# Optimization experiments

Measured on AMD Instinct MI355X. Metric: run time of the kernel, lower is better.

Reference implementation:

```python
import jax, jax.numpy as jnp
import numpy as np

N = 30000      # nodes
E = 480000     # edges (before self loops)
NFEAT = 128
H = 16         # heads
C = 32         # per-head channels = nhid
NCLASS = 10
G = 64         # graphs in batch
ATT_SLOPE = 0.2   # GATv2Conv negative_slope default
ACT_SLOPE = 0.01  # F.leaky_relu default


def setup_inputs() -> dict:
    key = jax.random.key(0)
    ks = jax.random.split(key, 16)
    def glorot(k, shape):
        fan = sum(shape[:2]) if len(shape) > 1 else shape[0]
        return jax.random.normal(k, shape, jnp.float32) * (2.0 / fan) ** 0.5
    inp = {
        "x": jax.random.normal(ks[0], (N, NFEAT), jnp.float32),
        # layer 1: lin_l / lin_r map NFEAT -> H*C, attention vector att [H, C]
        "Wl1": glorot(ks[1], (NFEAT, H * C)), "bl1": jnp.zeros((H * C,), jnp.float32),
        "Wr1": glorot(ks[2], (NFEAT, H * C)), "br1": jnp.zeros((H * C,), jnp.float32),
        "att1": glorot(ks[3], (H, C)), "b1": jnp.zeros((C,), jnp.float32),
        # layer 2: nhid(=C) -> H*C
        "Wl2": glorot(ks[4], (C, H * C)), "bl2": jnp.zeros((H * C,), jnp.float32),
        "Wr2": glorot(ks[5], (C, H * C)), "br2": jnp.zeros((H * C,), jnp.float32),
        "att2": glorot(ks[6], (H, C)), "b2": jnp.zeros((C,), jnp.float32),
        # classifier nhid -> nclass
        "Wc": glorot(ks[7], (C, NCLASS)), "bc": jnp.zeros((NCLASS,), jnp.float32),
        "edge_index": jax.random.randint(ks[8], (2, E), 0, N, jnp.int32),
        "batch": jnp.sort(jax.random.randint(ks[9], (N,), 0, G, jnp.int32)),
    }
    return inp


def _gatv2_layer(x, Wl, bl, Wr, br, att, b, src, dst, n):
    # GATv2Conv, concat=False (mean over heads), eval mode (no dropout)
    xl = (x @ Wl + bl).reshape(n, H, C)   # messages (x_j)
    xr = (x @ Wr + br).reshape(n, H, C)   # query side (x_i)
    e = jax.nn.leaky_relu(xl[src] + xr[dst], ATT_SLOPE)      # [E', H, C]
    score = jnp.einsum('ehc,hc->eh', e, att)                 # [E', H]
    # segment softmax over incoming edges of each dst node
    m = jax.ops.segment_max(score, dst, num_segments=n)
    ex = jnp.exp(score - m[dst])
    denom = jax.ops.segment_sum(ex, dst, num_segments=n)
    alpha = ex / denom[dst]                                  # [E', H]
    out = jax.ops.segment_sum(alpha[:, :, None] * xl[src], dst, num_segments=n)
    return out.mean(axis=1) + b                              # [n, C]


def reference(x, Wl1, bl1, Wr1, br1, att1, b1, Wl2, bl2, Wr2, br2, att2, b2, Wc, bc, edge_index, batch):
    # add self loops (PyG GATv2Conv default add_self_loops=True)
    loop = jnp.arange(N, dtype=edge_index.dtype)
    src = jnp.concatenate([edge_index[0], loop])
    dst = jnp.concatenate([edge_index[1], loop])

    h = jax.nn.leaky_relu(_gatv2_layer(x, Wl1, bl1, Wr1, br1, att1, b1, src, dst, N), ACT_SLOPE)
    h = jax.nn.leaky_relu(_gatv2_layer(h, Wl2, bl2, Wr2, br2, att2, b2, src, dst, N), ACT_SLOPE)
    # dropout is identity in eval mode
    # global mean pool over graphs
    summed = jax.ops.segment_sum(h, batch, num_segments=G)               # [G, C]
    counts = jax.ops.segment_sum(jnp.ones((N,), h.dtype), batch, num_segments=G)
    pooled = summed / jnp.maximum(counts, 1.0)[:, None]
    logits = pooled @ Wc + bc
    return logits / 1.0  # temperature = 1.0
```

## Files before the change

### kernel.cpp

```cpp
#include <hip/hip_runtime.h>
#include <float.h>

#define NNODES 30000
#define NEDGES 480000
#define NFEATK 128
#define NH 16
#define NC 32
#define HC 512
#define NCLASSES 10
#define NG 64
#define CAP 96

using half4 = __attribute__((ext_vector_type(4))) _Float16;
using half8 = __attribute__((ext_vector_type(8))) _Float16;
using f32x4 = __attribute__((ext_vector_type(4))) float;

__global__ void prep0_kernel(const float* __restrict__ x, _Float16* __restrict__ xh,
                             const float* __restrict__ Wl1, const float* __restrict__ Wr1,
                             _Float16* __restrict__ Wlt1, _Float16* __restrict__ Wrt1,
                             const float* __restrict__ Wl2, const float* __restrict__ Wr2,
                             _Float16* __restrict__ Wlt2, _Float16* __restrict__ Wrt2,
                             int* __restrict__ cnt, int* __restrict__ csr) {
    int gtid = blockIdx.x * blockDim.x + threadIdx.x;
    int gstride = gridDim.x * blockDim.x;
    for (int i = gtid; i < NNODES * NFEATK / 4; i += gstride) {
        float4 v = *(const float4*)&x[i * 4];
        half4 h = {(_Float16)v.x, (_Float16)v.y, (_Float16)v.z, (_Float16)v.w};
        *(half4*)&xh[i * 4] = h;
    }
    for (int i = gtid; i < 2 * 512 * NFEATK; i += gstride) {
        int sel = i >= 512 * NFEATK;
        int idx = i - sel * 512 * NFEATK;
        const float* W = sel ? Wr1 : Wl1;
        _Float16* Wt = sel ? Wrt1 : Wlt1;
        int n = idx & 511, k = idx >> 9;
        Wt[n * NFEATK + k] = (_Float16)W[idx];
    }
    for (int i = gtid; i < 2 * 512 * NC; i += gstride) {
        int sel = i >= 512 * NC;
        int idx = i - sel * 512 * NC;
        const float* W = sel ? Wr2 : Wl2;
        _Float16* Wt = sel ? Wrt2 : Wlt2;
        int n = idx & 511, k = idx >> 9;
        Wt[n * NC + k] = (_Float16)W[idx];
    }
    for (int i = gtid; i < NNODES; i += gstride) {
        cnt[i] = 1;
        csr[i * CAP] = i;
    }
}

__global__ void scatter_kernel(const int* __restrict__ src, const int* __restrict__ dst,
                               int* __restrict__ cnt, int* __restrict__ csr) {
    int e = blockIdx.x * blockDim.x + threadIdx.x;
    if (e >= NEDGES) return;
    int s = src[e], d = dst[e];
    int pos = atomicAdd(&cnt[d], 1);
    csr[d * CAP + pos] = s;
}

template <int K>
__launch_bounds__(256)
__global__ void dual_gemm_kernel(const _Float16* __restrict__ A,
                                 const _Float16* __restrict__ Wlt, const _Float16* __restrict__ Wrt,
                                 const float* __restrict__ bl, const float* __restrict__ br,
                                 _Float16* __restrict__ Yl, _Float16* __restrict__ Yr) {
    constexpr int Kc = K / 8;
    constexpr int AH = 64 * K;
    constexpr int BH = 128 * K;
    constexpr int YSH = 64 * 136;
    constexpr int SMEMH = (AH + BH > YSH) ? (AH + BH) : YSH;
    __shared__ __align__(16) _Float16 smem[SMEMH];
    _Float16* as = smem;
    _Float16* bs = smem + AH;

    int tid = threadIdx.x;
    int sel = blockIdx.y >> 2;
    int nbase = (blockIdx.y & 3) * 128;
    const _Float16* Bt = sel ? Wrt : Wlt;
    const float* bias = sel ? br : bl;
    _Float16* Y = sel ? Yr : Yl;
    int mb = blockIdx.x;

    for (int c = tid; c < 64 * Kc; c += 256) {
        int row = c / Kc, k8 = c % Kc;
        int arow = mb * 64 + row; if (arow > NNODES - 1) arow = NNODES - 1;
        half8 v = *(const half8*)&A[(size_t)arow * K + k8 * 8];
        *(half8*)&as[(row * Kc + (k8 ^ (row & (Kc - 1)))) * 8] = v;
    }
    for (int c = tid; c < 128 * Kc; c += 256) {
        int row = c / Kc, k8 = c % Kc;
        half8 v = *(const half8*)&Bt[(size_t)(nbase + row) * K + k8 * 8];
        *(half8*)&bs[(row * Kc + (k8 ^ (row & (Kc - 1)))) * 8] = v;
    }
    __syncthreads();

    int wave = tid >> 6, lane = tid & 63;
    int quad = lane >> 4, l16 = lane & 15;
    int am = l16 & (Kc - 1);

    f32x4 acc[8];
    #pragma unroll
    for (int f = 0; f < 8; f++) acc[f] = (f32x4){0.f, 0.f, 0.f, 0.f};

    #pragma unroll
    for (int kk = 0; kk < Kc; kk += 4) {
        int k8 = (kk + quad) ^ am;
        half8 a = *(const half8*)&as[((wave * 16 + l16) * Kc + k8) * 8];
        #pragma unroll
        for (int f = 0; f < 8; f++) {
            half8 b = *(const half8*)&bs[((f * 16 + l16) * Kc + k8) * 8];
            acc[f] = __builtin_amdgcn_mfma_f32_16x16x32_f16(a, b, acc[f], 0, 0, 0);
        }
    }
    __syncthreads();

    _Float16* ys = smem;
    #pragma unroll
    for (int f = 0; f < 8; f++) {
        float bv = bias[nbase + f * 16 + l16];
        #pragma unroll
        for (int r = 0; r < 4; r++) {
            ys[(wave * 16 + quad * 4 + r) * 136 + f * 16 + l16] = (_Float16)(acc[f][r] + bv);
        }
    }
    __syncthreads();
    int mtop = mb * 64;
    for (int c = tid; c < 64 * 16; c += 256) {
        int r = c >> 4, cc = (c & 15) * 8;
        int grow = mtop + r;
        if (grow < NNODES)
            *(half8*)&Y[(size_t)grow * HC + nbase + cc] = *(half8*)&ys[r * 136 + cc];
    }
}

template <typename OUT>
__launch_bounds__(128)
__global__ void gat_edge_kernel(const _Float16* __restrict__ xlh, const _Float16* __restrict__ xrh,
                                const float* __restrict__ att, const float* __restrict__ bvec,
                                const int* __restrict__ cnt, const int* __restrict__ csr_src,
                                OUT* __restrict__ hout) {
    int d = blockIdx.x;
    int t = threadIdx.x;
    int col = t * 4;
    half4 xrq = *(const half4*)&xrh[(size_t)d * HC + col];
    float4 xrv = {(float)xrq.x, (float)xrq.y, (float)xrq.z, (float)xrq.w};
    float4 attv = *(const float4*)&att[col];
    int beg = d * CAP, end = beg + cnt[d];

    float l = 0.f;
    float a0 = 0.f, a1 = 0.f, a2 = 0.f, a3 = 0.f;
    for (int i = beg; i < end; i += 4) {
        int n = end - i;
        int s0 = csr_src[i];
        int s1 = csr_src[n > 1 ? i + 1 : i];
        int s2 = csr_src[n > 2 ? i + 2 : i];
        int s3 = csr_src[n > 3 ? i + 3 : i];
        half4 q0 = *(const half4*)&xlh[(size_t)s0 * HC + col];
        half4 q1 = *(const half4*)&xlh[(size_t)s1 * HC + col];
        half4 q2 = *(const half4*)&xlh[(size_t)s2 * HC + col];
        half4 q3 = *(const half4*)&xlh[(size_t)s3 * HC + col];
        float x00 = (float)q0.x, x01 = (float)q0.y, x02 = (float)q0.z, x03 = (float)q0.w;
        float x10 = (float)q1.x, x11 = (float)q1.y, x12 = (float)q1.z, x13 = (float)q1.w;
        float x20 = (float)q2.x, x21 = (float)q2.y, x22 = (float)q2.z, x23 = (float)q2.w;
        float x30 = (float)q3.x, x31 = (float)q3.y, x32 = (float)q3.z, x33 = (float)q3.w;

        float e, v0, v1, v2, v3;
        e = x00 + xrv.x; e = (e > 0.f) ? e : 0.2f * e; v0  = e * attv.x;
        e = x01 + xrv.y; e = (e > 0.f) ? e : 0.2f * e; v0 += e * attv.y;
        e = x02 + xrv.z; e = (e > 0.f) ? e : 0.2f * e; v0 += e * attv.z;
        e = x03 + xrv.w; e = (e > 0.f) ? e : 0.2f * e; v0 += e * attv.w;
        e = x10 + xrv.x; e = (e > 0.f) ? e : 0.2f * e; v1  = e * attv.x;
        e = x11 + xrv.y; e = (e > 0.f) ? e : 0.2f * e; v1 += e * attv.y;
        e = x12 + xrv.z; e = (e > 0.f) ? e : 0.2f * e; v1 += e * attv.z;
        e = x13 + xrv.w; e = (e > 0.f) ? e : 0.2f * e; v1 += e * attv.w;
        e = x20 + xrv.x; e = (e > 0.f) ? e : 0.2f * e; v2  = e * attv.x;
        e = x21 + xrv.y; e = (e > 0.f) ? e : 0.2f * e; v2 += e * attv.y;
        e = x22 + xrv.z; e = (e > 0.f) ? e : 0.2f * e; v2 += e * attv.z;
        e = x23 + xrv.w; e = (e > 0.f) ? e : 0.2f * e; v2 += e * attv.w;
        e = x30 + xrv.x; e = (e > 0.f) ? e : 0.2f * e; v3  = e * attv.x;
        e = x31 + xrv.y; e = (e > 0.f) ? e : 0.2f * e; v3 += e * attv.y;
        e = x32 + xrv.z; e = (e > 0.f) ? e : 0.2f * e; v3 += e * attv.z;
        e = x33 + xrv.w; e = (e > 0.f) ? e : 0.2f * e; v3 += e * attv.w;

        #pragma unroll
        for (int off = 1; off < 8; off <<= 1) {
            v0 += __shfl_xor(v0, off);
            v1 += __shfl_xor(v1, off);
            v2 += __shfl_xor(v2, off);
            v3 += __shfl_xor(v3, off);
        }
        float p0 = __expf(v0);
        float p1 = (n > 1) ? __expf(v1) : 0.f;
        float p2 = (n > 2) ? __expf(v2) : 0.f;
        float p3 = (n > 3) ? __expf(v3) : 0.f;
        l += (p0 + p1) + (p2 + p3);
        a0 += p0 * x00 + p1 * x10 + p2 * x20 + p3 * x30;
        a1 += p0 * x01 + p1 * x11 + p2 * x21 + p3 * x31;
        a2 += p0 * x02 + p1 * x12 + p2 * x22 + p3 * x32;
        a3 += p0 * x03 + p1 * x13 + p2 * x23 + p3 * x33;
    }
    float inv = 1.0f / l;
    float4 o = {a0 * inv, a1 * inv, a2 * inv, a3 * inv};

    __shared__ float red[512];
    *(float4*)&red[col] = o;
    __syncthreads();
    if (t < 32) {
        float ssum = 0.f;
        #pragma unroll
        for (int hh = 0; hh < NH; ++hh) ssum += red[hh * 32 + t];
        float r = ssum * (1.0f / (float)NH) + bvec[t];
        r = (r > 0.f) ? r : 0.01f * r;
        hout[d * NC + t] = (OUT)r;
    }
}

__launch_bounds__(1024)
__global__ void pool_classify_kernel(const float* __restrict__ h, const int* __restrict__ batch,
                                     const float* __restrict__ Wc, const float* __restrict__ bc,
                                     float* __restrict__ out) {
    int g = blockIdx.x;
    int lo = 0, hi = NNODES;
    while (lo < hi) { int mid = (lo + hi) >> 1; if (batch[mid] < g) lo = mid + 1; else hi = mid; }
    int start = lo;
    hi = NNODES;
    while (lo < hi) { int mid = (lo + hi) >> 1; if (batch[mid] <= g) lo = mid + 1; else hi = mid; }
    int endn = lo;
    int cntg = endn - start;

    int tid = threadIdx.x;
    int c = tid & 31, nl = tid >> 5;
    float s = 0.f;
    for (int n = start + nl; n < endn; n += 32) s += h[n * NC + c];
    __shared__ float red[1024];
    red[tid] = s;
    __syncthreads();
    if (tid < 32) {
        float t = 0.f;
        #pragma unroll
        for (int j = 0; j < 32; j++) t += red[j * 32 + tid];
        red[tid] = t / fmaxf((float)cntg, 1.0f);
    }
    __syncthreads();
    if (tid < NCLASSES) {
        float sum = bc[tid];
        #pragma unroll
        for (int cc = 0; cc < NC; cc++) sum += red[cc] * Wc[cc * NCLASSES + tid];
        out[g * NCLASSES + tid] = sum;
    }
}


extern "C" void kernel_launch(void* const* d_in, const int* in_sizes, int n_in,
                              void* d_out, int out_size, void* d_ws, size_t ws_size,
                              hipStream_t stream) {
    const float* x    = (const float*)d_in[0];
    const float* Wl1  = (const float*)d_in[1];
    const float* bl1  = (const float*)d_in[2];
    const float* Wr1  = (const float*)d_in[3];
    const float* br1  = (const float*)d_in[4];
    const float* att1 = (const float*)d_in[5];
    const float* b1   = (const float*)d_in[6];
    const float* Wl2  = (const float*)d_in[7];
    const float* bl2  = (const float*)d_in[8];
    const float* Wr2  = (const float*)d_in[9];
    const float* br2  = (const float*)d_in[10];
    const float* att2 = (const float*)d_in[11];
    const float* b2   = (const float*)d_in[12];
    const float* Wc   = (const float*)d_in[13];
    const float* bc   = (const float*)d_in[14];
    const int* ei     = (const int*)d_in[15];
    const int* batch  = (const int*)d_in[16];
    float* out = (float*)d_out;

    const int* srcp = ei;
    const int* dstp = ei + NEDGES;

    char* ws = (char*)d_ws;
    size_t off = 0;
    auto alloc = [&](size_t bytes) -> void* {
        void* p = ws + off;
        off += (bytes + 255) & ~(size_t)255;
        return p;
    };
    _Float16* xlh  = (_Float16*)alloc(sizeof(_Float16) * (size_t)NNODES * HC);
    _Float16* xrh  = (_Float16*)alloc(sizeof(_Float16) * (size_t)NNODES * HC);
    _Float16* xh   = (_Float16*)alloc(sizeof(_Float16) * (size_t)NNODES * NFEATK);
    _Float16* h1   = (_Float16*)alloc(sizeof(_Float16) * (size_t)NNODES * NC);
    float* h2      = (float*)alloc(sizeof(float) * (size_t)NNODES * NC);
    _Float16* Wlt1 = (_Float16*)alloc(sizeof(_Float16) * 512 * NFEATK);
    _Float16* Wrt1 = (_Float16*)alloc(sizeof(_Float16) * 512 * NFEATK);
    _Float16* Wlt2 = (_Float16*)alloc(sizeof(_Float16) * 512 * NC);
    _Float16* Wrt2 = (_Float16*)alloc(sizeof(_Float16) * 512 * NC);
    int*   cnt     = (int*)alloc(sizeof(int) * NNODES);
    int*   csr     = (int*)alloc(sizeof(int) * (size_t)NNODES * CAP);

    prep0_kernel<<<512, 256, 0, stream>>>(x, xh, Wl1, Wr1, Wlt1, Wrt1,
                                          Wl2, Wr2, Wlt2, Wrt2, cnt, csr);
    scatter_kernel<<<(NEDGES + 255) / 256, 256, 0, stream>>>(srcp, dstp, cnt, csr);

    const int MB = (NNODES + 63) / 64;

    dual_gemm_kernel<NFEATK><<<dim3(MB, 8), 256, 0, stream>>>(xh, Wlt1, Wrt1, bl1, br1, xlh, xrh);
    gat_edge_kernel<_Float16><<<NNODES, 128, 0, stream>>>(xlh, xrh, att1, b1, cnt, csr, h1);

    dual_gemm_kernel<NC><<<dim3(MB, 8), 256, 0, stream>>>(h1, Wlt2, Wrt2, bl2, br2, xlh, xrh);
    gat_edge_kernel<float><<<NNODES, 128, 0, stream>>>(xlh, xrh, att2, b2, cnt, csr, h2);

    pool_classify_kernel<<<NG, 1024, 0, stream>>>(h2, batch, Wc, bc, out);
}
```

Measured before the change: 323.1 us.

## Merge edge scatter into prep, fold self-loops in-register, fuse pooling via atomics

```diff
diff --git a/kernel.cpp b/kernel.cpp
--- a/kernel.cpp
+++ b/kernel.cpp
@@ -11,18 +11,32 @@
 #define NG 64
 #define CAP 96
 
+#define CONV_BLOCKS 512
+#define SCAT_BLOCKS 1875
+
 using half4 = __attribute__((ext_vector_type(4))) _Float16;
 using half8 = __attribute__((ext_vector_type(8))) _Float16;
 using f32x4 = __attribute__((ext_vector_type(4))) float;
 
-__global__ void prep0_kernel(const float* __restrict__ x, _Float16* __restrict__ xh,
-                             const float* __restrict__ Wl1, const float* __restrict__ Wr1,
-                             _Float16* __restrict__ Wlt1, _Float16* __restrict__ Wrt1,
-                             const float* __restrict__ Wl2, const float* __restrict__ Wr2,
-                             _Float16* __restrict__ Wlt2, _Float16* __restrict__ Wrt2,
-                             int* __restrict__ cnt, int* __restrict__ csr) {
-    int gtid = blockIdx.x * blockDim.x + threadIdx.x;
-    int gstride = gridDim.x * blockDim.x;
+__global__ void prep_kernel(const float* __restrict__ x, _Float16* __restrict__ xh,
+                            const float* __restrict__ Wl1, const float* __restrict__ Wr1,
+                            _Float16* __restrict__ Wlt1, _Float16* __restrict__ Wrt1,
+                            const float* __restrict__ Wl2, const float* __restrict__ Wr2,
+                            _Float16* __restrict__ Wlt2, _Float16* __restrict__ Wrt2,
+                            const int* __restrict__ src, const int* __restrict__ dst,
+                            int* __restrict__ cnt, int* __restrict__ csr) {
+    int bid = blockIdx.x, tid = threadIdx.x;
+    if (bid >= CONV_BLOCKS) {
+        int e = (bid - CONV_BLOCKS) * 256 + tid;
+        if (e < NEDGES) {
+            int s = src[e], d = dst[e];
+            int pos = atomicAdd(&cnt[d], 1);
+            csr[d * CAP + pos] = s;
+        }
+        return;
+    }
+    int gtid = bid * 256 + tid;
+    const int gstride = CONV_BLOCKS * 256;
     for (int i = gtid; i < NNODES * NFEATK / 4; i += gstride) {
         float4 v = *(const float4*)&x[i * 4];
         half4 h = {(_Float16)v.x, (_Float16)v.y, (_Float16)v.z, (_Float16)v.w};
@@ -44,19 +58,6 @@
         int n = idx & 511, k = idx >> 9;
         Wt[n * NC + k] = (_Float16)W[idx];
     }
-    for (int i = gtid; i < NNODES; i += gstride) {
-        cnt[i] = 1;
-        csr[i * CAP] = i;
-    }
-}
-
-__global__ void scatter_kernel(const int* __restrict__ src, const int* __restrict__ dst,
-                               int* __restrict__ cnt, int* __restrict__ csr) {
-    int e = blockIdx.x * blockDim.x + threadIdx.x;
-    if (e >= NEDGES) return;
-    int s = src[e], d = dst[e];
-    int pos = atomicAdd(&cnt[d], 1);
-    csr[d * CAP + pos] = s;
 }
 
 template <int K>
@@ -134,12 +135,13 @@
     }
 }
 
-template <typename OUT>
+template <bool POOL, typename OUT>
 __launch_bounds__(128)
 __global__ void gat_edge_kernel(const _Float16* __restrict__ xlh, const _Float16* __restrict__ xrh,
                                 const float* __restrict__ att, const float* __restrict__ bvec,
                                 const int* __restrict__ cnt, const int* __restrict__ csr_src,
-                                OUT* __restrict__ hout) {
+                                const int* __restrict__ batch,
+                                OUT* __restrict__ hout, float* __restrict__ pool) {
     int d = blockIdx.x;
     int t = threadIdx.x;
     int col = t * 4;
@@ -148,8 +150,21 @@
     float4 attv = *(const float4*)&att[col];
     int beg = d * CAP, end = beg + cnt[d];
 
-    float l = 0.f;
-    float a0 = 0.f, a1 = 0.f, a2 = 0.f, a3 = 0.f;
+    float l, a0, a1, a2, a3;
+    {
+        half4 q = *(const half4*)&xlh[(size_t)d * HC + col];
+        float x0 = (float)q.x, x1 = (float)q.y, x2 = (float)q.z, x3 = (float)q.w;
+        float e, v;
+        e = x0 + xrv.x; e = (e > 0.f) ? e : 0.2f * e; v  = e * attv.x;
+        e = x1 + xrv.y; e = (e > 0.f) ? e : 0.2f * e; v += e * attv.y;
+        e = x2 + xrv.z; e = (e > 0.f) ? e : 0.2f * e; v += e * attv.z;
+        e = x3 + xrv.w; e = (e > 0.f) ? e : 0.2f * e; v += e * attv.w;
+        #pragma unroll
+        for (int off = 1; off < 8; off <<= 1) v += __shfl_xor(v, off);
+        float p = __expf(v);
+        l = p; a0 = p * x0; a1 = p * x1; a2 = p * x2; a3 = p * x3;
+    }
+
     for (int i = beg; i < end; i += 4) {
         int n = end - i;
         int s0 = csr_src[i];
@@ -212,43 +227,31 @@
         for (int hh = 0; hh < NH; ++hh) ssum += red[hh * 32 + t];
         float r = ssum * (1.0f / (float)NH) + bvec[t];
         r = (r > 0.f) ? r : 0.01f * r;
-        hout[d * NC + t] = (OUT)r;
-    }
-}
-
-__launch_bounds__(1024)
-__global__ void pool_classify_kernel(const float* __restrict__ h, const int* __restrict__ batch,
-                                     const float* __restrict__ Wc, const float* __restrict__ bc,
-                                     float* __restrict__ out) {
-    int g = blockIdx.x;
+        if constexpr (POOL) {
+            int g = batch[d];
+            atomicAdd(&pool[g * NC + t], r);
+        } else {
+            hout[d * NC + t] = (OUT)r;
+        }
+    }
+}
+
+__global__ void classify_kernel(const float* __restrict__ pool, const int* __restrict__ batch,
+                                const float* __restrict__ Wc, const float* __restrict__ bc,
+                                float* __restrict__ out) {
+    int t = blockIdx.x * blockDim.x + threadIdx.x;
+    if (t >= NG * NCLASSES) return;
+    int g = t / NCLASSES, k = t % NCLASSES;
     int lo = 0, hi = NNODES;
     while (lo < hi) { int mid = (lo + hi) >> 1; if (batch[mid] < g) lo = mid + 1; else hi = mid; }
     int start = lo;
     hi = NNODES;
     while (lo < hi) { int mid = (lo + hi) >> 1; if (batch[mid] <= g) lo = mid + 1; else hi = mid; }
-    int endn = lo;
-    int cntg = endn - start;
-
-    int tid = threadIdx.x;
-    int c = tid & 31, nl = tid >> 5;
-    float s = 0.f;
-    for (int n = start + nl; n < endn; n += 32) s += h[n * NC + c];
-    __shared__ float red[1024];
-    red[tid] = s;
-    __syncthreads();
-    if (tid < 32) {
-        float t = 0.f;
-        #pragma unroll
-        for (int j = 0; j < 32; j++) t += red[j * 32 + tid];
-        red[tid] = t / fmaxf((float)cntg, 1.0f);
-    }
-    __syncthreads();
-    if (tid < NCLASSES) {
-        float sum = bc[tid];
-        #pragma unroll
-        for (int cc = 0; cc < NC; cc++) sum += red[cc] * Wc[cc * NCLASSES + tid];
-        out[g * NCLASSES + tid] = sum;
-    }
+    float invc = 1.0f / fmaxf((float)(lo - start), 1.0f);
+    float sum = bc[k];
+    #pragma unroll
+    for (int c = 0; c < NC; c++) sum += pool[g * NC + c] * invc * Wc[c * NCLASSES + k];
+    out[g * NCLASSES + k] = sum;
 }
 
 
@@ -288,25 +291,28 @@
     _Float16* xrh  = (_Float16*)alloc(sizeof(_Float16) * (size_t)NNODES * HC);
     _Float16* xh   = (_Float16*)alloc(sizeof(_Float16) * (size_t)NNODES * NFEATK);
     _Float16* h1   = (_Float16*)alloc(sizeof(_Float16) * (size_t)NNODES * NC);
-    float* h2      = (float*)alloc(sizeof(float) * (size_t)NNODES * NC);
     _Float16* Wlt1 = (_Float16*)alloc(sizeof(_Float16) * 512 * NFEATK);
     _Float16* Wrt1 = (_Float16*)alloc(sizeof(_Float16) * 512 * NFEATK);
     _Float16* Wlt2 = (_Float16*)alloc(sizeof(_Float16) * 512 * NC);
     _Float16* Wrt2 = (_Float16*)alloc(sizeof(_Float16) * 512 * NC);
-    int*   cnt     = (int*)alloc(sizeof(int) * NNODES);
+    int*   cnt     = (int*)alloc(sizeof(int) * NNODES + sizeof(float) * NG * NC);
+    float* pool    = (float*)(cnt + NNODES);
     int*   csr     = (int*)alloc(sizeof(int) * (size_t)NNODES * CAP);
 
-    prep0_kernel<<<512, 256, 0, stream>>>(x, xh, Wl1, Wr1, Wlt1, Wrt1,
-                                          Wl2, Wr2, Wlt2, Wrt2, cnt, csr);
-    scatter_kernel<<<(NEDGES + 255) / 256, 256, 0, stream>>>(srcp, dstp, cnt, csr);
+    hipMemsetAsync(cnt, 0, sizeof(int) * NNODES + sizeof(float) * NG * NC, stream);
+
+    prep_kernel<<<CONV_BLOCKS + SCAT_BLOCKS, 256, 0, stream>>>(
+        x, xh, Wl1, Wr1, Wlt1, Wrt1, Wl2, Wr2, Wlt2, Wrt2, srcp, dstp, cnt, csr);
 
     const int MB = (NNODES + 63) / 64;
 
     dual_gemm_kernel<NFEATK><<<dim3(MB, 8), 256, 0, stream>>>(xh, Wlt1, Wrt1, bl1, br1, xlh, xrh);
-    gat_edge_kernel<_Float16><<<NNODES, 128, 0, stream>>>(xlh, xrh, att1, b1, cnt, csr, h1);
+    gat_edge_kernel<false, _Float16><<<NNODES, 128, 0, stream>>>(
+        xlh, xrh, att1, b1, cnt, csr, batch, h1, nullptr);
 
     dual_gemm_kernel<NC><<<dim3(MB, 8), 256, 0, stream>>>(h1, Wlt2, Wrt2, bl2, br2, xlh, xrh);
-    gat_edge_kernel<float><<<NNODES, 128, 0, stream>>>(xlh, xrh, att2, b2, cnt, csr, h2);
-
-    pool_classify_kernel<<<NG, 1024, 0, stream>>>(h2, batch, Wc, bc, out);
-}
+    gat_edge_kernel<true, float><<<NNODES, 128, 0, stream>>>(
+        xlh, xrh, att2, b2, cnt, csr, batch, (float*)nullptr, pool);
+
+    classify_kernel<<<(NG * NCLASSES + 255) / 256, 256, 0, stream>>>(pool, batch, Wc, bc, out);
+}
```

After: 336.2 us. 1.04x slower.

## Fuse input fp16 conversion and edge scatter into first GEMM launch

Applied to the files above, without the earlier changes.

```diff
diff --git a/kernel.cpp b/kernel.cpp
--- a/kernel.cpp
+++ b/kernel.cpp
@@ -11,23 +11,20 @@
 #define NG 64
 #define CAP 96
 
+#define MBP 472
+#define GEMM_BLOCKS (MBP * 8)
+#define SCAT_BLOCKS 1875
+
 using half4 = __attribute__((ext_vector_type(4))) _Float16;
 using half8 = __attribute__((ext_vector_type(8))) _Float16;
 using f32x4 = __attribute__((ext_vector_type(4))) float;
 
-__global__ void prep0_kernel(const float* __restrict__ x, _Float16* __restrict__ xh,
-                             const float* __restrict__ Wl1, const float* __restrict__ Wr1,
+__global__ void wconv_kernel(const float* __restrict__ Wl1, const float* __restrict__ Wr1,
+                             const float* __restrict__ Wl2, const float* __restrict__ Wr2,
                              _Float16* __restrict__ Wlt1, _Float16* __restrict__ Wrt1,
-                             const float* __restrict__ Wl2, const float* __restrict__ Wr2,
-                             _Float16* __restrict__ Wlt2, _Float16* __restrict__ Wrt2,
-                             int* __restrict__ cnt, int* __restrict__ csr) {
+                             _Float16* __restrict__ Wlt2, _Float16* __restrict__ Wrt2) {
     int gtid = blockIdx.x * blockDim.x + threadIdx.x;
     int gstride = gridDim.x * blockDim.x;
-    for (int i = gtid; i < NNODES * NFEATK / 4; i += gstride) {
-        float4 v = *(const float4*)&x[i * 4];
-        half4 h = {(_Float16)v.x, (_Float16)v.y, (_Float16)v.z, (_Float16)v.w};
-        *(half4*)&xh[i * 4] = h;
-    }
     for (int i = gtid; i < 2 * 512 * NFEATK; i += gstride) {
         int sel = i >= 512 * NFEATK;
         int idx = i - sel * 512 * NFEATK;
@@ -44,27 +41,16 @@
         int n = idx & 511, k = idx >> 9;
         Wt[n * NC + k] = (_Float16)W[idx];
     }
-    for (int i = gtid; i < NNODES; i += gstride) {
-        cnt[i] = 1;
-        csr[i * CAP] = i;
-    }
-}
-
-__global__ void scatter_kernel(const int* __restrict__ src, const int* __restrict__ dst,
-                               int* __restrict__ cnt, int* __restrict__ csr) {
-    int e = blockIdx.x * blockDim.x + threadIdx.x;
-    if (e >= NEDGES) return;
-    int s = src[e], d = dst[e];
-    int pos = atomicAdd(&cnt[d], 1);
-    csr[d * CAP + pos] = s;
-}
-
-template <int K>
+}
+
+template <int K, bool CONVA, bool SCATTER>
 __launch_bounds__(256)
-__global__ void dual_gemm_kernel(const _Float16* __restrict__ A,
+__global__ void dual_gemm_kernel(const void* __restrict__ Avoid,
                                  const _Float16* __restrict__ Wlt, const _Float16* __restrict__ Wrt,
                                  const float* __restrict__ bl, const float* __restrict__ br,
-                                 _Float16* __restrict__ Yl, _Float16* __restrict__ Yr) {
+                                 _Float16* __restrict__ Yl, _Float16* __restrict__ Yr,
+                                 const int* __restrict__ src, const int* __restrict__ dst,
+                                 int* __restrict__ cnt, int* __restrict__ csr) {
     constexpr int Kc = K / 8;
     constexpr int AH = 64 * K;
     constexpr int BH = 128 * K;
@@ -74,18 +60,40 @@
     _Float16* as = smem;
     _Float16* bs = smem + AH;
 
-    int tid = threadIdx.x;
-    int sel = blockIdx.y >> 2;
-    int nbase = (blockIdx.y & 3) * 128;
+    int bid = blockIdx.x, tid = threadIdx.x;
+    if constexpr (SCATTER) {
+        if (bid >= GEMM_BLOCKS) {
+            int e = (bid - GEMM_BLOCKS) * 256 + tid;
+            if (e < NEDGES) {
+                int s = src[e], d = dst[e];
+                int pos = atomicAdd(&cnt[d], 1);
+                csr[d * CAP + pos] = s;
+            }
+            return;
+        }
+    }
+    int mb = bid % MBP;
+    int yy = bid / MBP;
+    if (mb * 64 >= NNODES) return;
+    int sel = yy >> 2;
+    int nbase = (yy & 3) * 128;
     const _Float16* Bt = sel ? Wrt : Wlt;
     const float* bias = sel ? br : bl;
     _Float16* Y = sel ? Yr : Yl;
-    int mb = blockIdx.x;
 
     for (int c = tid; c < 64 * Kc; c += 256) {
         int row = c / Kc, k8 = c % Kc;
         int arow = mb * 64 + row; if (arow > NNODES - 1) arow = NNODES - 1;
-        half8 v = *(const half8*)&A[(size_t)arow * K + k8 * 8];
+        half8 v;
+        if constexpr (CONVA) {
+            const float* xp = (const float*)Avoid + (size_t)arow * K + k8 * 8;
+            float4 f0 = *(const float4*)xp;
+            float4 f1 = *(const float4*)(xp + 4);
+            v = half8{(_Float16)f0.x, (_Float16)f0.y, (_Float16)f0.z, (_Float16)f0.w,
+                      (_Float16)f1.x, (_Float16)f1.y, (_Float16)f1.z, (_Float16)f1.w};
+        } else {
+            v = *(const half8*)((const _Float16*)Avoid + (size_t)arow * K + k8 * 8);
+        }
         *(half8*)&as[(row * Kc + (k8 ^ (row & (Kc - 1)))) * 8] = v;
     }
     for (int c = tid; c < 128 * Kc; c += 256) {
@@ -148,8 +156,21 @@
     float4 attv = *(const float4*)&att[col];
     int beg = d * CAP, end = beg + cnt[d];
 
-    float l = 0.f;
-    float a0 = 0.f, a1 = 0.f, a2 = 0.f, a3 = 0.f;
+    float l, a0, a1, a2, a3;
+    {
+        half4 q = *(const half4*)&xlh[(size_t)d * HC + col];
+        float x0 = (float)q.x, x1 = (float)q.y, x2 = (float)q.z, x3 = (float)q.w;
+        float e, v;
+        e = x0 + xrv.x; e = (e > 0.f) ? e : 0.2f * e; v  = e * attv.x;
+        e = x1 + xrv.y; e = (e > 0.f) ? e : 0.2f * e; v += e * attv.y;
+        e = x2 + xrv.z; e = (e > 0.f) ? e : 0.2f * e; v += e * attv.z;
+        e = x3 + xrv.w; e = (e > 0.f) ? e : 0.2f * e; v += e * attv.w;
+        #pragma unroll
+        for (int off = 1; off < 8; off <<= 1) v += __shfl_xor(v, off);
+        float p = __expf(v);
+        l = p; a0 = p * x0; a1 = p * x1; a2 = p * x2; a3 = p * x3;
+    }
+
     for (int i = beg; i < end; i += 4) {
         int n = end - i;
         int s0 = csr_src[i];
@@ -286,7 +307,6 @@
     };
     _Float16* xlh  = (_Float16*)alloc(sizeof(_Float16) * (size_t)NNODES * HC);
     _Float16* xrh  = (_Float16*)alloc(sizeof(_Float16) * (size_t)NNODES * HC);
-    _Float16* xh   = (_Float16*)alloc(sizeof(_Float16) * (size_t)NNODES * NFEATK);
     _Float16* h1   = (_Float16*)alloc(sizeof(_Float16) * (size_t)NNODES * NC);
     float* h2      = (float*)alloc(sizeof(float) * (size_t)NNODES * NC);
     _Float16* Wlt1 = (_Float16*)alloc(sizeof(_Float16) * 512 * NFEATK);
@@ -296,16 +316,16 @@
     int*   cnt     = (int*)alloc(sizeof(int) * NNODES);
     int*   csr     = (int*)alloc(sizeof(int) * (size_t)NNODES * CAP);
 
-    prep0_kernel<<<512, 256, 0, stream>>>(x, xh, Wl1, Wr1, Wlt1, Wrt1,
-                                          Wl2, Wr2, Wlt2, Wrt2, cnt, csr);
-    scatter_kernel<<<(NEDGES + 255) / 256, 256, 0, stream>>>(srcp, dstp, cnt, csr);
-
-    const int MB = (NNODES + 63) / 64;
-
-    dual_gemm_kernel<NFEATK><<<dim3(MB, 8), 256, 0, stream>>>(xh, Wlt1, Wrt1, bl1, br1, xlh, xrh);
+    hipMemsetAsync(cnt, 0, sizeof(int) * NNODES, stream);
+
+    wconv_kernel<<<320, 256, 0, stream>>>(Wl1, Wr1, Wl2, Wr2, Wlt1, Wrt1, Wlt2, Wrt2);
+
+    dual_gemm_kernel<NFEATK, true, true><<<GEMM_BLOCKS + SCAT_BLOCKS, 256, 0, stream>>>(
+        x, Wlt1, Wrt1, bl1, br1, xlh, xrh, srcp, dstp, cnt, csr);
     gat_edge_kernel<_Float16><<<NNODES, 128, 0, stream>>>(xlh, xrh, att1, b1, cnt, csr, h1);
 
-    dual_gemm_kernel<NC><<<dim3(MB, 8), 256, 0, stream>>>(h1, Wlt2, Wrt2, bl2, br2, xlh, xrh);
+    dual_gemm_kernel<NC, false, false><<<GEMM_BLOCKS, 256, 0, stream>>>(
+        h1, Wlt2, Wrt2, bl2, br2, xlh, xrh, nullptr, nullptr, nullptr, nullptr);
     gat_edge_kernel<float><<<NNODES, 128, 0, stream>>>(xlh, xrh, att2, b2, cnt, csr, h2);
 
     pool_classify_kernel<<<NG, 1024, 0, stream>>>(h2, batch, Wc, bc, out);
```

New measurement: 324.1 us. No clear change (+0.3%).
